# Optimization experiments

Measured on AMD Instinct MI355X. Metric: run time of the kernel, lower is better.

The kernel has to match this reference:

```python
import math
import jax, jax.numpy as jnp
import numpy as np

D_HIDDEN, D_MODEL, SEQ_LEN = 2048, 4096, 4096
R_MIN, R_MAX, MAX_PHASE = 0.0, 1.0, 6.28


def setup_inputs() -> dict:
    key = jax.random.key(0)
    ks = jax.random.split(key, 8)
    # nu_log / theta_log per the LRU stable-ring init
    u1 = jax.random.uniform(ks[0], (D_HIDDEN,))
    nu_log = jnp.log(-0.5 * jnp.log(u1 * (R_MAX ** 2 - R_MIN ** 2) + R_MIN ** 2))
    u2 = jax.random.uniform(ks[1], (D_HIDDEN,))
    theta_log = jnp.log(MAX_PHASE * u2)
    diag_lambda = jnp.exp(-jnp.exp(nu_log) + 1j * jnp.exp(theta_log))
    gamma_log = jnp.log(jnp.sqrt(1.0 - jnp.abs(diag_lambda) ** 2))
    B_re = jax.random.normal(ks[2], (D_HIDDEN, D_MODEL)) / math.sqrt(2 * D_MODEL)
    B_im = jax.random.normal(ks[3], (D_HIDDEN, D_MODEL)) / math.sqrt(2 * D_MODEL)
    C_re = jax.random.normal(ks[4], (D_MODEL, D_HIDDEN)) / math.sqrt(D_HIDDEN)
    C_im = jax.random.normal(ks[5], (D_MODEL, D_HIDDEN)) / math.sqrt(D_HIDDEN)
    D = jax.random.normal(ks[6], (D_MODEL,))
    inputs = jax.random.normal(ks[7], (SEQ_LEN, D_MODEL), dtype=jnp.float32)
    return {
        "inputs": inputs,
        "nu_log": nu_log,
        "theta_log": theta_log,
        "gamma_log": gamma_log,
        "B_re": B_re,
        "B_im": B_im,
        "C_re": C_re,
        "C_im": C_im,
        "D": D,
    }


def reference(inputs, nu_log, theta_log, gamma_log, B_re, B_im, C_re, C_im, D):
    x = inputs.astype(jnp.complex64)
    # Diagonal complex recurrence matrix
    diag_lambda = jnp.exp(-jnp.exp(nu_log) + 1j * jnp.exp(theta_log))  # (H,)
    B_norm = (B_re + 1j * B_im) * jnp.exp(gamma_log)[:, None]          # (H, D)
    Bu = jnp.einsum('hd,td->th', B_norm, x)                            # (T, H)
    Lam = jnp.broadcast_to(diag_lambda, Bu.shape)                       # (T, H)

    # h_t = lambda * h_{t-1} + Bu_t  via log-depth associative scan
    def op(a, b):
        return (a[0] * b[0], b[0] * a[1] + b[1])

    _, hidden = jax.lax.associative_scan(op, (Lam, Bu))                 # (T, H)

    C = C_re + 1j * C_im                                                # (D, H)
    outputs = jnp.matmul(hidden, C.T).real + inputs * D                 # (T, D)
    return outputs.astype(jnp.float32)
```

## Files before the change

### kernel.cpp

```cpp
#include <hip/hip_runtime.h>
#include <hip/hip_bf16.h>

typedef unsigned short u16;
typedef float f32x4 __attribute__((ext_vector_type(4)));
typedef __bf16 bf16x8 __attribute__((ext_vector_type(8)));

constexpr int TSEQ = 4096;
constexpr int DMOD = 4096;
constexpr int HID  = 2048;
constexpr int HID2 = 4096;
constexpr int NCH  = 64;
constexpr int CHL  = 64;

__device__ __forceinline__ u16 f2bf(float f) {
  unsigned u = __builtin_bit_cast(unsigned, f);
  u += 0x7fffu + ((u >> 16) & 1u);
  return (u16)(u >> 16);
}
__device__ __forceinline__ unsigned pack2(float a, float b) {
  return (unsigned)f2bf(a) | ((unsigned)f2bf(b) << 16);
}
__device__ __forceinline__ void load_lds16(const u16* g, u16* l) {
  __builtin_amdgcn_global_load_lds((const __attribute__((address_space(1))) void*)g,
                                   (__attribute__((address_space(3))) void*)l,
                                   16, 0, 0);
}
__device__ __forceinline__ unsigned lds_addr(const u16* p) {
  return (unsigned)(uintptr_t)(const __attribute__((address_space(3))) u16*)p;
}

__global__ __launch_bounds__(256) void k_lambda(const float* __restrict__ nu_log,
                                                const float* __restrict__ theta_log,
                                                float* __restrict__ lam_re, float* __restrict__ lam_im,
                                                float* __restrict__ lamL_re, float* __restrict__ lamL_im) {
  int h = blockIdx.x * 256 + threadIdx.x;
  if (h >= HID) return;
  float nu = expf(nu_log[h]);
  float th = expf(theta_log[h]);
  float mag = expf(-nu);
  float lr = mag * cosf(th), li = mag * sinf(th);
  lam_re[h] = lr; lam_im[h] = li;
  float pr = lr, pi = li;
#pragma unroll
  for (int i = 0; i < 6; ++i) {
    float nr = pr * pr - pi * pi;
    float ni = 2.f * pr * pi;
    pr = nr; pi = ni;
  }
  lamL_re[h] = pr; lamL_im[h] = pi;
}

__global__ __launch_bounds__(256) void k_cast_x(const float* __restrict__ x, u16* __restrict__ xb) {
  size_t i = ((size_t)blockIdx.x * 256 + threadIdx.x) * 4;
  float4 v = *reinterpret_cast<const float4*>(x + i);
  uint2 o;
  o.x = pack2(v.x, v.y);
  o.y = pack2(v.z, v.w);
  *reinterpret_cast<uint2*>(xb + i) = o;
}

__global__ __launch_bounds__(256) void k_make_bcat(const float* __restrict__ Bre, const float* __restrict__ Bim,
                                                   const float* __restrict__ gamma_log, u16* __restrict__ Bcat) {
  int idx = blockIdx.x * 256 + threadIdx.x;
  int h  = idx / (DMOD / 4);
  int dv = (idx % (DMOD / 4)) * 4;
  float g = expf(gamma_log[h]);
  float4 r  = *reinterpret_cast<const float4*>(Bre + (size_t)h * DMOD + dv);
  float4 im = *reinterpret_cast<const float4*>(Bim + (size_t)h * DMOD + dv);
  uint2 orr; orr.x = pack2(r.x * g, r.y * g); orr.y = pack2(r.z * g, r.w * g);
  *reinterpret_cast<uint2*>(Bcat + (size_t)h * DMOD + dv) = orr;
  uint2 oim; oim.x = pack2(im.x * g, im.y * g); oim.y = pack2(im.z * g, im.w * g);
  *reinterpret_cast<uint2*>(Bcat + (size_t)(h + HID) * DMOD + dv) = oim;
}

__global__ __launch_bounds__(256) void k_make_ccat(const float* __restrict__ Cre, const float* __restrict__ Cim,
                                                   u16* __restrict__ Ccat) {
  int idx = blockIdx.x * 256 + threadIdx.x;
  int d  = idx / (HID / 4);
  int hv = (idx % (HID / 4)) * 4;
  float4 r  = *reinterpret_cast<const float4*>(Cre + (size_t)d * HID + hv);
  float4 im = *reinterpret_cast<const float4*>(Cim + (size_t)d * HID + hv);
  uint2 orr; orr.x = pack2(r.x, r.y); orr.y = pack2(r.z, r.w);
  *reinterpret_cast<uint2*>(Ccat + (size_t)d * HID2 + hv) = orr;
  uint2 oim; oim.x = pack2(-im.x, -im.y); oim.y = pack2(-im.z, -im.w);
  *reinterpret_cast<uint2*>(Ccat + (size_t)d * HID2 + HID + hv) = oim;
}

#define DSR(d, a, IMM) asm volatile("ds_read_b128 %0, %1 offset:" IMM : "=v"(d) : "v"(a))

#define RD_A(B, O0, O1, O2, O3) do { \
  DSR(af[0][0], aAk0[B], O0); DSR(af[0][1], aAk1[B], O0); \
  DSR(af[1][0], aAk0[B], O1); DSR(af[1][1], aAk1[B], O1); \
  DSR(af[2][0], aAk0[B], O2); DSR(af[2][1], aAk1[B], O2); \
  DSR(af[3][0], aAk0[B], O3); DSR(af[3][1], aAk1[B], O3); } while (0)

#define RD_B(B, DST, O0, O1) do { \
  DSR(DST[0][0], aBk0[B], O0); DSR(DST[0][1], aBk1[B], O0); \
  DSR(DST[1][0], aBk0[B], O1); DSR(DST[1][1], aBk1[B], O1); } while (0)

#define STAGE_A(b, h, kb) do { const u16* _s = stA + (size_t)(h) * 128 * 4096 + (kb); \
  load_lds16(_s, dA[b][h]); load_lds16(_s + 64 * 4096, dA[b][h] + 4096); } while (0)
#define STAGE_B(b, h, kb) do { const u16* _s = stB + (size_t)(h) * 128 * 4096 + (kb); \
  load_lds16(_s, dB[b][h]); load_lds16(_s + 64 * 4096, dB[b][h] + 4096); } while (0)

#define MMQ(MB, NB, BF) do { \
  _Pragma("unroll") for (int m = 0; m < 4; ++m) { \
  _Pragma("unroll") for (int n = 0; n < 2; ++n) { \
    acc[(MB)+m][(NB)+n] = __builtin_amdgcn_mfma_f32_16x16x32_bf16(af[m][0], BF[n][0], acc[(MB)+m][(NB)+n], 0, 0, 0); \
    acc[(MB)+m][(NB)+n] = __builtin_amdgcn_mfma_f32_16x16x32_bf16(af[m][1], BF[n][1], acc[(MB)+m][(NB)+n], 0, 0, 0); } } } while (0)

#define MID() do { __builtin_amdgcn_s_barrier(); \
  asm volatile("s_waitcnt lgkmcnt(0)"); \
  __builtin_amdgcn_sched_barrier(0); \
  __builtin_amdgcn_s_setprio(1); } while (0)
#define ENDP() do { __builtin_amdgcn_s_setprio(0); \
  __builtin_amdgcn_s_barrier(); } while (0)
#define ENDPV() do { __builtin_amdgcn_s_setprio(0); \
  asm volatile("s_waitcnt vmcnt(4)"); \
  __builtin_amdgcn_s_barrier(); } while (0)

template <bool EPI>
__global__ __launch_bounds__(512, 2) void gemm8(const u16* __restrict__ A, const u16* __restrict__ Bt,
                                                float* __restrict__ C,
                                                const float* __restrict__ resid,
                                                const float* __restrict__ dvec) {
  constexpr int K = 4096, N = 4096;
  constexpr int NI = (K / 64) / 2;
  __shared__ __align__(16) u16 L[65536];

  int nwg = gridDim.x;
  int wg = blockIdx.x;
  wg = (wg & 7) * (nwg >> 3) + (wg >> 3);
  int bm = (wg >> 4) << 8;
  int bn = (wg & 15) << 8;

  int tid = threadIdx.x;
  int lane = tid & 63;
  int wave = tid >> 6;
  int wm = wave >> 2, wn = wave & 3;
  int l15 = lane & 15, g = lane >> 4;

  unsigned offk0 = (unsigned)(((unsigned)g << 4) ^ ((unsigned)(lane & 7) << 4));
  unsigned offk1 = offk0 ^ 64u;
  unsigned aAk0[2], aAk1[2], aBk0[2], aBk1[2];
#pragma unroll
  for (int b = 0; b < 2; ++b) {
    unsigned ab = lds_addr(&L[b * 32768 + wm * 8192 + l15 * 64]);
    aAk0[b] = ab + offk0; aAk1[b] = ab + offk1;
    unsigned bb = lds_addr(&L[b * 32768 + 16384 + (wn >> 1) * 8192 + (wn & 1) * 4096 + l15 * 64]);
    aBk0[b] = bb + offk0; aBk1[b] = bb + offk1;
  }

  int trow = tid >> 3;
  int tchk = ((tid & 7) ^ (trow & 7)) << 3;
  const u16* stA = A  + (size_t)(bm + trow) * K + tchk;
  const u16* stB = Bt + (size_t)(bn + trow) * K + tchk;
  u16* dA[2][2]; u16* dB[2][2];
#pragma unroll
  for (int b = 0; b < 2; ++b)
#pragma unroll
    for (int h = 0; h < 2; ++h) {
      dA[b][h] = &L[b * 32768 + h * 8192 + tid * 8];
      dB[b][h] = &L[b * 32768 + 16384 + h * 8192 + tid * 8];
    }

  bf16x8 af[4][2], b0[2][2], b1[2][2];
  f32x4 acc[8][4];
#pragma unroll
  for (int i = 0; i < 8; ++i)
#pragma unroll
    for (int n = 0; n < 4; ++n) acc[i][n] = (f32x4){0.f, 0.f, 0.f, 0.f};

  STAGE_B(0, 0, 0);  STAGE_A(0, 0, 0);
  STAGE_B(0, 1, 0);  STAGE_A(0, 1, 0);
  STAGE_B(1, 0, 64); STAGE_A(1, 0, 64);
  asm volatile("s_waitcnt vmcnt(4)");
  __builtin_amdgcn_s_barrier();

#pragma unroll 1
  for (int j = 0; j < NI; ++j) {
    int kb1 = ((2 * j + 1) << 6) & (K - 1);
    int kb2 = ((2 * j + 2) << 6) & (K - 1);
    int kb3 = ((2 * j + 3) << 6) & (K - 1);
    RD_A(0, "0", "2048", "4096", "6144");
    RD_B(0, b0, "0", "2048");
    STAGE_B(1, 1, kb1);
    MID(); MMQ(0, 0, b0); ENDP();
    RD_B(0, b1, "4096", "6144");
    STAGE_A(1, 1, kb1);
    MID(); MMQ(0, 2, b1); ENDP();
    RD_A(0, "8192", "10240", "12288", "14336");
    STAGE_B(0, 0, kb2);
    MID(); MMQ(4, 2, b1); ENDP();
    STAGE_A(0, 0, kb2);
    MID(); MMQ(4, 0, b0); ENDPV();
    RD_A(1, "0", "2048", "4096", "6144");
    RD_B(1, b0, "0", "2048");
    STAGE_B(0, 1, kb2);
    MID(); MMQ(0, 0, b0); ENDP();
    RD_B(1, b1, "4096", "6144");
    STAGE_A(0, 1, kb2);
    MID(); MMQ(0, 2, b1); ENDP();
    RD_A(1, "8192", "10240", "12288", "14336");
    STAGE_B(1, 0, kb3);
    MID(); MMQ(4, 2, b1); ENDP();
    STAGE_A(1, 0, kb3);
    MID(); MMQ(4, 0, b0); ENDPV();
  }

  int crow = bm + wm * 128 + (g << 2);
  int ccol = bn + wn * 64 + l15;
#pragma unroll
  for (int mi = 0; mi < 8; ++mi)
#pragma unroll
    for (int ni = 0; ni < 4; ++ni)
#pragma unroll
      for (int jj = 0; jj < 4; ++jj) {
        int row = crow + mi * 16 + jj;
        int col = ccol + ni * 16;
        float v = acc[mi][ni][jj];
        if constexpr (EPI) v += resid[(size_t)row * N + col] * dvec[col];
        C[(size_t)row * N + col] = v;
      }
}

__global__ __launch_bounds__(256) void s_chunk_end(const float* __restrict__ Bu,
                                                   const float* __restrict__ lam_re,
                                                   const float* __restrict__ lam_im,
                                                   float* __restrict__ E) {
  int t = blockIdx.x * 256 + threadIdx.x;
  int h = t & (HID - 1);
  int c = t >> 11;
  float lr = lam_re[h], li = lam_im[h];
  float sr = 0.f, si = 0.f;
  const float* base = Bu + (size_t)c * CHL * HID2;
#pragma unroll 4
  for (int i = 0; i < CHL; ++i) {
    float br = base[(size_t)i * HID2 + h];
    float bi = base[(size_t)i * HID2 + HID + h];
    float nr = lr * sr - li * si + br;
    float ni = lr * si + li * sr + bi;
    sr = nr; si = ni;
  }
  E[(size_t)c * HID + h] = sr;
  E[(size_t)NCH * HID + (size_t)c * HID + h] = si;
}

__global__ __launch_bounds__(256) void s_prefix(const float* __restrict__ lamL_re,
                                                const float* __restrict__ lamL_im,
                                                const float* __restrict__ E,
                                                float* __restrict__ P) {
  int h = blockIdx.x * 256 + threadIdx.x;
  if (h >= HID) return;
  float plr = lamL_re[h], pli = lamL_im[h];
  float pr = 0.f, pi = 0.f;
  for (int c = 0; c < NCH; ++c) {
    P[(size_t)c * HID + h] = pr;
    P[(size_t)NCH * HID + (size_t)c * HID + h] = pi;
    float er = E[(size_t)c * HID + h];
    float ei = E[(size_t)NCH * HID + (size_t)c * HID + h];
    float nr = plr * pr - pli * pi + er;
    float ni = plr * pi + pli * pr + ei;
    pr = nr; pi = ni;
  }
}

__global__ __launch_bounds__(256) void s_expand(const float* __restrict__ Bu,
                                                const float* __restrict__ lam_re,
                                                const float* __restrict__ lam_im,
                                                const float* __restrict__ P,
                                                u16* __restrict__ A2) {
  int t = blockIdx.x * 256 + threadIdx.x;
  int h = t & (HID - 1);
  int c = t >> 11;
  float lr = lam_re[h], li = lam_im[h];
  float sr = P[(size_t)c * HID + h];
  float si = P[(size_t)NCH * HID + (size_t)c * HID + h];
  const float* base = Bu + (size_t)c * CHL * HID2;
  u16* ob = A2 + (size_t)c * CHL * HID2;
#pragma unroll 4
  for (int i = 0; i < CHL; ++i) {
    float br = base[(size_t)i * HID2 + h];
    float bi = base[(size_t)i * HID2 + HID + h];
    float nr = lr * sr - li * si + br;
    float ni = lr * si + li * sr + bi;
    sr = nr; si = ni;
    ob[(size_t)i * HID2 + h]       = f2bf(sr);
    ob[(size_t)i * HID2 + HID + h] = f2bf(si);
  }
}

extern "C" void kernel_launch(void* const* d_in, const int* in_sizes, int n_in,
                              void* d_out, int out_size, void* d_ws, size_t ws_size,
                              hipStream_t stream) {
  const float* inputs    = (const float*)d_in[0];
  const float* nu_log    = (const float*)d_in[1];
  const float* theta_log = (const float*)d_in[2];
  const float* gamma_log = (const float*)d_in[3];
  const float* B_re      = (const float*)d_in[4];
  const float* B_im      = (const float*)d_in[5];
  const float* C_re      = (const float*)d_in[6];
  const float* C_im      = (const float*)d_in[7];
  const float* Dvec      = (const float*)d_in[8];

  char* w = (char*)d_ws;
  u16* xb     = (u16*)w;
  u16* Bcat   = (u16*)(w + (size_t)33554432);
  float* lam_re  = (float*)(w + (size_t)67108864);
  float* lam_im  = lam_re + HID;
  float* lamL_re = lam_im + HID;
  float* lamL_im = lamL_re + HID;
  float* E       = lamL_im + HID;
  float* P       = E + (size_t)NCH * HID * 2;

  float* Bu  = (float*)d_out;
  float* out = (float*)d_out;

  k_lambda<<<dim3(HID / 256), dim3(256), 0, stream>>>(nu_log, theta_log, lam_re, lam_im, lamL_re, lamL_im);
  k_cast_x<<<dim3((TSEQ * DMOD / 4) / 256), dim3(256), 0, stream>>>(inputs, xb);
  k_make_bcat<<<dim3((HID * DMOD / 4) / 256), dim3(256), 0, stream>>>(B_re, B_im, gamma_log, Bcat);

  gemm8<false><<<dim3((TSEQ / 256) * (HID2 / 256)), dim3(512), 0, stream>>>(
      xb, Bcat, Bu, nullptr, nullptr);

  s_chunk_end<<<dim3(NCH * HID / 256), dim3(256), 0, stream>>>(Bu, lam_re, lam_im, E);
  s_prefix<<<dim3(HID / 256), dim3(256), 0, stream>>>(lamL_re, lamL_im, E, P);
  s_expand<<<dim3(NCH * HID / 256), dim3(256), 0, stream>>>(Bu, lam_re, lam_im, P, xb );

  k_make_ccat<<<dim3((DMOD * HID / 4) / 256), dim3(256), 0, stream>>>(C_re, C_im, Bcat );

  gemm8<true><<<dim3((TSEQ / 256) * (DMOD / 256)), dim3(512), 0, stream>>>(
      xb , Bcat , out, inputs, Dvec);
}
```

Before: 480.6 us.

## Store Bu intermediate as bf16 and vectorize scan kernels over four channels

The first GEMM now writes its Bu output as bf16 instead of fp32, which halves the write traffic and the reads in both scan passes. The chunk-end and expand scan kernels each handle four hidden channels per thread with 8-byte vector loads and stores, launching a quarter as many threads. The MFMA loop order in MMQ is reordered so that k is the outer loop, and the prefix loop is unrolled. The cost is extra rounding of Bu before the recurrence, and fewer threads in the scans means less parallelism to hide latency.

```diff
diff --git a/kernel.cpp b/kernel.cpp
--- a/kernel.cpp
+++ b/kernel.cpp
@@ -16,6 +16,9 @@
   unsigned u = __builtin_bit_cast(unsigned, f);
   u += 0x7fffu + ((u >> 16) & 1u);
   return (u16)(u >> 16);
+}
+__device__ __forceinline__ float bf2f(u16 u) {
+  return __builtin_bit_cast(float, (unsigned)u << 16);
 }
 __device__ __forceinline__ unsigned pack2(float a, float b) {
   return (unsigned)f2bf(a) | ((unsigned)f2bf(b) << 16);
@@ -104,10 +107,10 @@
   load_lds16(_s, dB[b][h]); load_lds16(_s + 64 * 4096, dB[b][h] + 4096); } while (0)
 
 #define MMQ(MB, NB, BF) do { \
+  _Pragma("unroll") for (int k = 0; k < 2; ++k) { \
   _Pragma("unroll") for (int m = 0; m < 4; ++m) { \
   _Pragma("unroll") for (int n = 0; n < 2; ++n) { \
-    acc[(MB)+m][(NB)+n] = __builtin_amdgcn_mfma_f32_16x16x32_bf16(af[m][0], BF[n][0], acc[(MB)+m][(NB)+n], 0, 0, 0); \
-    acc[(MB)+m][(NB)+n] = __builtin_amdgcn_mfma_f32_16x16x32_bf16(af[m][1], BF[n][1], acc[(MB)+m][(NB)+n], 0, 0, 0); } } } while (0)
+    acc[(MB)+m][(NB)+n] = __builtin_amdgcn_mfma_f32_16x16x32_bf16(af[m][k], BF[n][k], acc[(MB)+m][(NB)+n], 0, 0, 0); } } } } while (0)
 
 #define MID() do { __builtin_amdgcn_s_barrier(); \
   asm volatile("s_waitcnt lgkmcnt(0)"); \
@@ -121,7 +124,7 @@
 
 template <bool EPI>
 __global__ __launch_bounds__(512, 2) void gemm8(const u16* __restrict__ A, const u16* __restrict__ Bt,
-                                                float* __restrict__ C,
+                                                void* __restrict__ Cout,
                                                 const float* __restrict__ resid,
                                                 const float* __restrict__ dvec) {
   constexpr int K = 4096, N = 4096;
@@ -219,31 +222,44 @@
         int row = crow + mi * 16 + jj;
         int col = ccol + ni * 16;
         float v = acc[mi][ni][jj];
-        if constexpr (EPI) v += resid[(size_t)row * N + col] * dvec[col];
-        C[(size_t)row * N + col] = v;
+        if constexpr (EPI) {
+          v += resid[(size_t)row * N + col] * dvec[col];
+          ((float*)Cout)[(size_t)row * N + col] = v;
+        } else {
+          ((u16*)Cout)[(size_t)row * N + col] = f2bf(v);
+        }
       }
 }
 
-__global__ __launch_bounds__(256) void s_chunk_end(const float* __restrict__ Bu,
+__global__ __launch_bounds__(256) void s_chunk_end(const u16* __restrict__ Bu,
                                                    const float* __restrict__ lam_re,
                                                    const float* __restrict__ lam_im,
                                                    float* __restrict__ E) {
   int t = blockIdx.x * 256 + threadIdx.x;
-  int h = t & (HID - 1);
-  int c = t >> 11;
-  float lr = lam_re[h], li = lam_im[h];
-  float sr = 0.f, si = 0.f;
-  const float* base = Bu + (size_t)c * CHL * HID2;
-#pragma unroll 4
+  int hq = t & (HID / 4 - 1);
+  int c  = t >> 9;
+  int h0 = hq << 2;
+  float4 lr = *reinterpret_cast<const float4*>(lam_re + h0);
+  float4 li = *reinterpret_cast<const float4*>(lam_im + h0);
+  float sr[4] = {0.f, 0.f, 0.f, 0.f}, si[4] = {0.f, 0.f, 0.f, 0.f};
+  const float lrv[4] = {lr.x, lr.y, lr.z, lr.w};
+  const float liv[4] = {li.x, li.y, li.z, li.w};
+  const u16* base = Bu + (size_t)c * CHL * HID2 + h0;
+#pragma unroll 8
   for (int i = 0; i < CHL; ++i) {
-    float br = base[(size_t)i * HID2 + h];
-    float bi = base[(size_t)i * HID2 + HID + h];
-    float nr = lr * sr - li * si + br;
-    float ni = lr * si + li * sr + bi;
-    sr = nr; si = ni;
-  }
-  E[(size_t)c * HID + h] = sr;
-  E[(size_t)NCH * HID + (size_t)c * HID + h] = si;
+    ushort4 vre = *reinterpret_cast<const ushort4*>(base + (size_t)i * HID2);
+    ushort4 vim = *reinterpret_cast<const ushort4*>(base + (size_t)i * HID2 + HID);
+    float br[4] = {bf2f(vre.x), bf2f(vre.y), bf2f(vre.z), bf2f(vre.w)};
+    float bi[4] = {bf2f(vim.x), bf2f(vim.y), bf2f(vim.z), bf2f(vim.w)};
+#pragma unroll
+    for (int q = 0; q < 4; ++q) {
+      float nr = lrv[q] * sr[q] - liv[q] * si[q] + br[q];
+      float ni = lrv[q] * si[q] + liv[q] * sr[q] + bi[q];
+      sr[q] = nr; si[q] = ni;
+    }
+  }
+  *reinterpret_cast<float4*>(E + (size_t)c * HID + h0) = (float4){sr[0], sr[1], sr[2], sr[3]};
+  *reinterpret_cast<float4*>(E + (size_t)NCH * HID + (size_t)c * HID + h0) = (float4){si[0], si[1], si[2], si[3]};
 }
 
 __global__ __launch_bounds__(256) void s_prefix(const float* __restrict__ lamL_re,
@@ -254,6 +270,7 @@
   if (h >= HID) return;
   float plr = lamL_re[h], pli = lamL_im[h];
   float pr = 0.f, pi = 0.f;
+#pragma unroll
   for (int c = 0; c < NCH; ++c) {
     P[(size_t)c * HID + h] = pr;
     P[(size_t)NCH * HID + (size_t)c * HID + h] = pi;
@@ -265,28 +282,40 @@
   }
 }
 
-__global__ __launch_bounds__(256) void s_expand(const float* __restrict__ Bu,
+__global__ __launch_bounds__(256) void s_expand(const u16* __restrict__ Bu,
                                                 const float* __restrict__ lam_re,
                                                 const float* __restrict__ lam_im,
                                                 const float* __restrict__ P,
                                                 u16* __restrict__ A2) {
   int t = blockIdx.x * 256 + threadIdx.x;
-  int h = t & (HID - 1);
-  int c = t >> 11;
-  float lr = lam_re[h], li = lam_im[h];
-  float sr = P[(size_t)c * HID + h];
-  float si = P[(size_t)NCH * HID + (size_t)c * HID + h];
-  const float* base = Bu + (size_t)c * CHL * HID2;
-  u16* ob = A2 + (size_t)c * CHL * HID2;
-#pragma unroll 4
+  int hq = t & (HID / 4 - 1);
+  int c  = t >> 9;
+  int h0 = hq << 2;
+  float4 lr = *reinterpret_cast<const float4*>(lam_re + h0);
+  float4 li = *reinterpret_cast<const float4*>(lam_im + h0);
+  const float lrv[4] = {lr.x, lr.y, lr.z, lr.w};
+  const float liv[4] = {li.x, li.y, li.z, li.w};
+  float4 p0 = *reinterpret_cast<const float4*>(P + (size_t)c * HID + h0);
+  float4 p1 = *reinterpret_cast<const float4*>(P + (size_t)NCH * HID + (size_t)c * HID + h0);
+  float sr[4] = {p0.x, p0.y, p0.z, p0.w}, si[4] = {p1.x, p1.y, p1.z, p1.w};
+  const u16* base = Bu + (size_t)c * CHL * HID2 + h0;
+  u16* ob = A2 + (size_t)c * CHL * HID2 + h0;
+#pragma unroll 8
   for (int i = 0; i < CHL; ++i) {
-    float br = base[(size_t)i * HID2 + h];
-    float bi = base[(size_t)i * HID2 + HID + h];
-    float nr = lr * sr - li * si + br;
-    float ni = lr * si + li * sr + bi;
-    sr = nr; si = ni;
-    ob[(size_t)i * HID2 + h]       = f2bf(sr);
-    ob[(size_t)i * HID2 + HID + h] = f2bf(si);
+    ushort4 vre = *reinterpret_cast<const ushort4*>(base + (size_t)i * HID2);
+    ushort4 vim = *reinterpret_cast<const ushort4*>(base + (size_t)i * HID2 + HID);
+    float br[4] = {bf2f(vre.x), bf2f(vre.y), bf2f(vre.z), bf2f(vre.w)};
+    float bi[4] = {bf2f(vim.x), bf2f(vim.y), bf2f(vim.z), bf2f(vim.w)};
+#pragma unroll
+    for (int q = 0; q < 4; ++q) {
+      float nr = lrv[q] * sr[q] - liv[q] * si[q] + br[q];
+      float ni = lrv[q] * si[q] + liv[q] * sr[q] + bi[q];
+      sr[q] = nr; si[q] = ni;
+    }
+    ushort4 ore = {f2bf(sr[0]), f2bf(sr[1]), f2bf(sr[2]), f2bf(sr[3])};
+    ushort4 oim = {f2bf(si[0]), f2bf(si[1]), f2bf(si[2]), f2bf(si[3])};
+    *reinterpret_cast<ushort4*>(ob + (size_t)i * HID2) = ore;
+    *reinterpret_cast<ushort4*>(ob + (size_t)i * HID2 + HID) = oim;
   }
 }
 
@@ -313,7 +342,7 @@
   float* E       = lamL_im + HID;
   float* P       = E + (size_t)NCH * HID * 2;
 
-  float* Bu  = (float*)d_out;
+  u16* Bu    = (u16*)d_out;
   float* out = (float*)d_out;
 
   k_lambda<<<dim3(HID / 256), dim3(256), 0, stream>>>(nu_log, theta_log, lam_re, lam_im, lamL_re, lamL_im);
@@ -321,14 +350,14 @@
   k_make_bcat<<<dim3((HID * DMOD / 4) / 256), dim3(256), 0, stream>>>(B_re, B_im, gamma_log, Bcat);
 
   gemm8<false><<<dim3((TSEQ / 256) * (HID2 / 256)), dim3(512), 0, stream>>>(
-      xb, Bcat, Bu, nullptr, nullptr);
-
-  s_chunk_end<<<dim3(NCH * HID / 256), dim3(256), 0, stream>>>(Bu, lam_re, lam_im, E);
+      xb, Bcat, (void*)Bu, nullptr, nullptr);
+
+  s_chunk_end<<<dim3(NCH * HID / 4 / 256), dim3(256), 0, stream>>>(Bu, lam_re, lam_im, E);
   s_prefix<<<dim3(HID / 256), dim3(256), 0, stream>>>(lamL_re, lamL_im, E, P);
-  s_expand<<<dim3(NCH * HID / 256), dim3(256), 0, stream>>>(Bu, lam_re, lam_im, P, xb );
+  s_expand<<<dim3(NCH * HID / 4 / 256), dim3(256), 0, stream>>>(Bu, lam_re, lam_im, P, xb );
 
   k_make_ccat<<<dim3((DMOD * HID / 4) / 256), dim3(256), 0, stream>>>(C_re, C_im, Bcat );
 
   gemm8<true><<<dim3((TSEQ / 256) * (DMOD / 256)), dim3(512), 0, stream>>>(
-      xb , Bcat , out, inputs, Dvec);
-}
+      xb , Bcat , (void*)out, inputs, Dvec);
+}
```

Result: no change. 478.8 us (-0.4%).
